# Optimization experiments

Hardware: AMD Instinct MI355X
Metric: run time of the kernel (lower is better)

## Reference

```python
import jax, jax.numpy as jnp
import numpy as np

N = 500_000
B = 4096
H = 256
NH = 4
D = H // NH


def setup_inputs() -> dict:
    key = jax.random.key(0)
    ks = jax.random.split(key, 9)
    node_feats = jax.random.normal(ks[0], (N, H), dtype=jnp.float32)
    g_feats = jax.random.normal(ks[1], (B, H), dtype=jnp.float32)
    degree = jax.random.uniform(ks[2], (N, 1), dtype=jnp.float32)
    seg = jnp.sort(jax.random.randint(ks[3], (N,), 0, B, dtype=jnp.int32))
    attn = jax.random.normal(ks[4], (1, NH, D), dtype=jnp.float32) * 0.1
    W1 = jax.random.normal(ks[5], (H, H), dtype=jnp.float32) * (1.0 / np.sqrt(H))
    b1 = jnp.zeros((H,), dtype=jnp.float32)
    W2 = jax.random.normal(ks[6], (H, H), dtype=jnp.float32) * (1.0 / np.sqrt(H))
    b2 = jnp.zeros((H,), dtype=jnp.float32)
    return {"node_feats": node_feats, "g_feats": g_feats, "degree": degree,
            "seg": seg, "attn": attn, "W1": W1, "b1": b1, "W2": W2, "b2": b2}


def reference(node_feats, g_feats, degree, seg, attn, W1, b1, W2, b2):
    nB, nH = g_feats.shape
    nD = nH // NH
    # broadcast graph feats to nodes + residual, split into heads: [N, NH, D]
    hv = (g_feats[seg] + node_feats).reshape(-1, NH, nD)
    # attention score per node per head: [N, NH]
    z = jnp.einsum('nhd,ohd->nh', hv, attn)
    z = z * degree  # degree [N,1] broadcasts over heads
    # per-graph (segment) softmax over nodes, per head
    zmax = jax.ops.segment_max(z, seg, num_segments=nB)  # [B, NH]
    zmax = jnp.where(jnp.isfinite(zmax), zmax, 0.0)       # guard empty graphs
    e = jnp.exp(z - zmax[seg])
    denom = jax.ops.segment_sum(e, seg, num_segments=nB)  # [B, NH]
    a = e / jnp.maximum(denom[seg], 1e-12)                 # [N, NH]
    # weighted segment sum of hv: [B, NH, D] -> [B, H]
    he = jax.ops.segment_sum(hv * a[:, :, None], seg, num_segments=nB)
    he = he.reshape(nB, nH)
    # lin1 (ReLU) then lin2 (no act), residual with g_feats
    h1 = jax.nn.relu(he @ W1.T + b1)
    h2 = h1 @ W2.T + b2
    return h2 + g_feats
```

## Files before the change

### kernel.cpp

```cpp
#include <hip/hip_runtime.h>
#include <math.h>

#define H 256
#define NHD 4
#define BM 8

typedef float f32x4 __attribute__((ext_vector_type(4)));

__global__ void transpose2_kernel(const float* __restrict__ W1,
                                  const float* __restrict__ W2,
                                  float* __restrict__ W1T,
                                  float* __restrict__ W2T) {
    __shared__ float tile[32][33];
    const int which = blockIdx.x >> 6;
    const float* in = which ? W2 : W1;
    float* out = which ? W2T : W1T;
    const int blk = blockIdx.x & 63;
    const int bx = blk & 7, by = blk >> 3;
    const int tx = threadIdx.x & 31, ty = threadIdx.x >> 5;
#pragma unroll
    for (int r = 0; r < 32; r += 8)
        tile[ty + r][tx] = in[(by * 32 + ty + r) * H + bx * 32 + tx];
    __syncthreads();
#pragma unroll
    for (int r = 0; r < 32; r += 8)
        out[(bx * 32 + ty + r) * H + by * 32 + tx] = tile[tx][ty + r];
}

__launch_bounds__(256, 8)
__global__ void pool_kernel(const float* __restrict__ node_feats,
                            const float* __restrict__ g_feats,
                            const float* __restrict__ degree,
                            const float* __restrict__ attn,
                            const int* __restrict__ seg,
                            int N,
                            float* __restrict__ he_out) {
    const int b = blockIdx.x;
    const int tid = threadIdx.x;
    const int wave = tid >> 6;
    const int lane = tid & 63;

    __shared__ int sb[2];
    if (tid < 2) {
        const int target = b + tid;
        int lo = 0, hi = N;
        while (lo < hi) {
            int mid = (lo + hi) >> 1;
            if (seg[mid] < target) lo = mid + 1; else hi = mid;
        }
        sb[tid] = lo;
    }
    __syncthreads();
    const int start = sb[0];
    const int end = sb[1];

    const float4 g4 = *reinterpret_cast<const float4*>(g_feats + (size_t)b * H + lane * 4);
    const float4 a4 = *reinterpret_cast<const float4*>(attn + lane * 4);

    float gz = g4.x * a4.x + g4.y * a4.y + g4.z * a4.z + g4.w * a4.w;
#pragma unroll
    for (int s = 1; s < 16; s <<= 1) gz += __shfl_xor(gz, s, 64);

    float m = -INFINITY, lsum = 0.0f;
    float4 acc = make_float4(0.f, 0.f, 0.f, 0.f);

    int n0 = start + wave * 4;
    for (; n0 + 4 <= end; n0 += 16) {
        const float* rp = node_feats + (size_t)n0 * H + lane * 4;
        f32x4 v0 = __builtin_nontemporal_load(reinterpret_cast<const f32x4*>(rp));
        f32x4 v1 = __builtin_nontemporal_load(reinterpret_cast<const f32x4*>(rp + H));
        f32x4 v2 = __builtin_nontemporal_load(reinterpret_cast<const f32x4*>(rp + 2 * H));
        f32x4 v3 = __builtin_nontemporal_load(reinterpret_cast<const f32x4*>(rp + 3 * H));
        const float d0 = degree[n0], d1 = degree[n0 + 1];
        const float d2 = degree[n0 + 2], d3 = degree[n0 + 3];

        float p0 = v0[0] * a4.x + v0[1] * a4.y + v0[2] * a4.z + v0[3] * a4.w;
        float p1 = v1[0] * a4.x + v1[1] * a4.y + v1[2] * a4.z + v1[3] * a4.w;
        float p2 = v2[0] * a4.x + v2[1] * a4.y + v2[2] * a4.z + v2[3] * a4.w;
        float p3 = v3[0] * a4.x + v3[1] * a4.y + v3[2] * a4.z + v3[3] * a4.w;
#pragma unroll
        for (int s = 1; s < 16; s <<= 1) {
            p0 += __shfl_xor(p0, s, 64);
            p1 += __shfl_xor(p1, s, 64);
            p2 += __shfl_xor(p2, s, 64);
            p3 += __shfl_xor(p3, s, 64);
        }
        const float z0 = (p0 + gz) * d0, z1 = (p1 + gz) * d1;
        const float z2 = (p2 + gz) * d2, z3 = (p3 + gz) * d3;

        const float mz = fmaxf(fmaxf(z0, z1), fmaxf(z2, z3));
        const float e0 = __expf(z0 - mz), e1 = __expf(z1 - mz);
        const float e2 = __expf(z2 - mz), e3 = __expf(z3 - mz);
        const float ls = e0 + e1 + e2 + e3;
        const float ax = e0 * v0[0] + e1 * v1[0] + e2 * v2[0] + e3 * v3[0] + ls * g4.x;
        const float ay = e0 * v0[1] + e1 * v1[1] + e2 * v2[1] + e3 * v3[1] + ls * g4.y;
        const float az = e0 * v0[2] + e1 * v1[2] + e2 * v2[2] + e3 * v3[2] + ls * g4.z;
        const float aw = e0 * v0[3] + e1 * v1[3] + e2 * v2[3] + e3 * v3[3] + ls * g4.w;

        const float mnew = fmaxf(m, mz);
        const float fo = __expf(m - mnew);
        const float fn = __expf(mz - mnew);
        lsum = lsum * fo + ls * fn;
        acc.x = acc.x * fo + ax * fn;
        acc.y = acc.y * fo + ay * fn;
        acc.z = acc.z * fo + az * fn;
        acc.w = acc.w * fo + aw * fn;
        m = mnew;
    }
    const int nend = (n0 + 4 < end) ? (n0 + 4) : end;
    for (int n = n0; n < nend; ++n) {
        const float* rp = node_feats + (size_t)n * H + lane * 4;
        f32x4 v = __builtin_nontemporal_load(reinterpret_cast<const f32x4*>(rp));
        float p = v[0] * a4.x + v[1] * a4.y + v[2] * a4.z + v[3] * a4.w;
#pragma unroll
        for (int s = 1; s < 16; s <<= 1) p += __shfl_xor(p, s, 64);
        const float z = (p + gz) * degree[n];
        const float mnew = fmaxf(m, z);
        const float fo = __expf(m - mnew);
        const float e = __expf(z - mnew);
        lsum = lsum * fo + e;
        acc.x = acc.x * fo + e * (v[0] + g4.x);
        acc.y = acc.y * fo + e * (v[1] + g4.y);
        acc.z = acc.z * fo + e * (v[2] + g4.z);
        acc.w = acc.w * fo + e * (v[3] + g4.w);
        m = mnew;
    }

    __shared__ float sm[4][NHD];
    __shared__ float sl[4][NHD];
    __shared__ float sacc[4][H];
    const int head = lane >> 4;
    if ((lane & 15) == 0) { sm[wave][head] = m; sl[wave][head] = lsum; }
    *reinterpret_cast<float4*>(&sacc[wave][lane * 4]) = acc;
    __syncthreads();

    const int h = tid >> 6;
    float mstar = fmaxf(fmaxf(sm[0][h], sm[1][h]), fmaxf(sm[2][h], sm[3][h]));
    if (!(mstar > -INFINITY)) mstar = 0.0f;
    float denom = 0.0f, hev = 0.0f;
#pragma unroll
    for (int w = 0; w < 4; ++w) {
        float fw = __expf(sm[w][h] - mstar);
        denom += sl[w][h] * fw;
        hev += sacc[w][tid] * fw;
    }
    he_out[(size_t)b * H + tid] = hev / fmaxf(denom, 1e-12f);
}

__launch_bounds__(256, 4)
__global__ void mlp_kernel(const float* __restrict__ he,
                           const float* __restrict__ W1T,
                           const float* __restrict__ b1,
                           const float* __restrict__ W2T,
                           const float* __restrict__ b2,
                           const float* __restrict__ g_feats,
                           float* __restrict__ out) {
    __shared__ float hbuf[BM][H];
    __shared__ float h1buf[BM][H];
    const int tid = threadIdx.x;
    const size_t row0 = (size_t)blockIdx.x * BM;

#pragma unroll
    for (int i = 0; i < BM; ++i)
        hbuf[i][tid] = he[(row0 + i) * H + tid];
    __syncthreads();

    float acc[BM];
#pragma unroll
    for (int i = 0; i < BM; ++i) acc[i] = 0.f;
    for (int k = 0; k < H; k += 4) {
        float w0 = W1T[(size_t)(k + 0) * H + tid];
        float w1 = W1T[(size_t)(k + 1) * H + tid];
        float w2 = W1T[(size_t)(k + 2) * H + tid];
        float w3 = W1T[(size_t)(k + 3) * H + tid];
#pragma unroll
        for (int i = 0; i < BM; ++i) {
            float4 hv = *reinterpret_cast<const float4*>(&hbuf[i][k]);
            acc[i] += hv.x * w0 + hv.y * w1 + hv.z * w2 + hv.w * w3;
        }
    }
    float bb1 = b1[tid];
#pragma unroll
    for (int i = 0; i < BM; ++i) h1buf[i][tid] = fmaxf(acc[i] + bb1, 0.f);
    __syncthreads();

#pragma unroll
    for (int i = 0; i < BM; ++i) acc[i] = 0.f;
    for (int k = 0; k < H; k += 4) {
        float w0 = W2T[(size_t)(k + 0) * H + tid];
        float w1 = W2T[(size_t)(k + 1) * H + tid];
        float w2 = W2T[(size_t)(k + 2) * H + tid];
        float w3 = W2T[(size_t)(k + 3) * H + tid];
#pragma unroll
        for (int i = 0; i < BM; ++i) {
            float4 hv = *reinterpret_cast<const float4*>(&h1buf[i][k]);
            acc[i] += hv.x * w0 + hv.y * w1 + hv.z * w2 + hv.w * w3;
        }
    }
    float bb2 = b2[tid];
#pragma unroll
    for (int i = 0; i < BM; ++i)
        out[(row0 + i) * H + tid] = acc[i] + bb2 + g_feats[(row0 + i) * H + tid];
}

extern "C" void kernel_launch(void* const* d_in, const int* in_sizes, int n_in,
                              void* d_out, int out_size, void* d_ws, size_t ws_size,
                              hipStream_t stream) {
    const float* node_feats = (const float*)d_in[0];
    const float* g_feats    = (const float*)d_in[1];
    const float* degree     = (const float*)d_in[2];
    const int*   seg        = (const int*)d_in[3];
    const float* attn       = (const float*)d_in[4];
    const float* W1         = (const float*)d_in[5];
    const float* b1         = (const float*)d_in[6];
    const float* W2         = (const float*)d_in[7];
    const float* b2         = (const float*)d_in[8];
    float* out = (float*)d_out;

    const int N = in_sizes[3];
    const int B = in_sizes[1] / H;

    char* ws = (char*)d_ws;
    float* W1T = (float*)ws;
    float* W2T = (float*)(ws + H * H * 4);
    float* he  = (float*)(ws + 2 * H * H * 4);

    transpose2_kernel<<<128, 256, 0, stream>>>(W1, W2, W1T, W2T);
    pool_kernel<<<B, 256, 0, stream>>>(node_feats, g_feats, degree, attn, seg, N, he);
    mlp_kernel<<<B / BM, 256, 0, stream>>>(he, W1T, b1, W2T, b2, g_feats, out);
}
```

Before: 139.1 us.

## Precompute segment bounds in a separate kernel and split-K the MLP across waves

Adds a kernel that writes per-graph start offsets from the sorted segment ids, so each pool block reads two integers instead of running two serial binary searches before any work. The MLP kernel now gives each wave a quarter of the K dimension and has each thread compute four output columns, then reduces the partial sums through shared memory. The goal is more register-level reuse of the loaded weights and more independent FMA chains. The cost is an extra launch, a larger shared-memory buffer and an added reduction step with barriers.

```diff
diff --git a/kernel.cpp b/kernel.cpp
--- a/kernel.cpp
+++ b/kernel.cpp
@@ -6,6 +6,23 @@
 #define BM 8
 
 typedef float f32x4 __attribute__((ext_vector_type(4)));
+
+__global__ void seg_bounds_kernel(const int* __restrict__ seg,
+                                  int* __restrict__ seg_start,
+                                  int N, int B) {
+    int n = blockIdx.x * blockDim.x + threadIdx.x;
+    if (n >= N) return;
+    int s = seg[n];
+    if (n == 0) {
+        for (int b = 0; b <= s; ++b) seg_start[b] = 0;
+    } else {
+        int sp = seg[n - 1];
+        for (int b = sp + 1; b <= s; ++b) seg_start[b] = n;
+    }
+    if (n == N - 1) {
+        for (int b = s + 1; b <= B; ++b) seg_start[b] = N;
+    }
+}
 
 __global__ void transpose2_kernel(const float* __restrict__ W1,
                                   const float* __restrict__ W2,
@@ -32,27 +49,14 @@
                             const float* __restrict__ g_feats,
                             const float* __restrict__ degree,
                             const float* __restrict__ attn,
-                            const int* __restrict__ seg,
-                            int N,
+                            const int* __restrict__ seg_start,
                             float* __restrict__ he_out) {
     const int b = blockIdx.x;
     const int tid = threadIdx.x;
     const int wave = tid >> 6;
     const int lane = tid & 63;
-
-    __shared__ int sb[2];
-    if (tid < 2) {
-        const int target = b + tid;
-        int lo = 0, hi = N;
-        while (lo < hi) {
-            int mid = (lo + hi) >> 1;
-            if (seg[mid] < target) lo = mid + 1; else hi = mid;
-        }
-        sb[tid] = lo;
-    }
-    __syncthreads();
-    const int start = sb[0];
-    const int end = sb[1];
+    const int start = seg_start[b];
+    const int end = seg_start[b + 1];
 
     const float4 g4 = *reinterpret_cast<const float4*>(g_feats + (size_t)b * H + lane * 4);
     const float4 a4 = *reinterpret_cast<const float4*>(attn + lane * 4);
@@ -156,8 +160,10 @@
                            const float* __restrict__ g_feats,
                            float* __restrict__ out) {
     __shared__ float hbuf[BM][H];
-    __shared__ float h1buf[BM][H];
+    __shared__ float pacc[4][BM][H];
     const int tid = threadIdx.x;
+    const int q = tid >> 6;
+    const int l = tid & 63;
     const size_t row0 = (size_t)blockIdx.x * BM;
 
 #pragma unroll
@@ -165,42 +171,62 @@
         hbuf[i][tid] = he[(row0 + i) * H + tid];
     __syncthreads();
 
-    float acc[BM];
-#pragma unroll
-    for (int i = 0; i < BM; ++i) acc[i] = 0.f;
-    for (int k = 0; k < H; k += 4) {
-        float w0 = W1T[(size_t)(k + 0) * H + tid];
-        float w1 = W1T[(size_t)(k + 1) * H + tid];
-        float w2 = W1T[(size_t)(k + 2) * H + tid];
-        float w3 = W1T[(size_t)(k + 3) * H + tid];
-#pragma unroll
-        for (int i = 0; i < BM; ++i) {
-            float4 hv = *reinterpret_cast<const float4*>(&hbuf[i][k]);
-            acc[i] += hv.x * w0 + hv.y * w1 + hv.z * w2 + hv.w * w3;
+#pragma unroll
+    for (int layer = 0; layer < 2; ++layer) {
+        const float* WT = layer ? W2T : W1T;
+        float acc[BM][4];
+#pragma unroll
+        for (int i = 0; i < BM; ++i)
+#pragma unroll
+            for (int j = 0; j < 4; ++j) acc[i][j] = 0.f;
+
+        const int k0 = q * 64;
+        for (int s = 0; s < 64; s += 4) {
+            const int k = k0 + s;
+            float w[4][4];
+#pragma unroll
+            for (int kk = 0; kk < 4; ++kk)
+#pragma unroll
+                for (int j = 0; j < 4; ++j)
+                    w[kk][j] = WT[(size_t)(k + kk) * H + l + 64 * j];
+#pragma unroll
+            for (int i = 0; i < BM; ++i) {
+                const f32x4 hv = *reinterpret_cast<const f32x4*>(&hbuf[i][k]);
+#pragma unroll
+                for (int j = 0; j < 4; ++j) {
+                    acc[i][j] = __builtin_fmaf(hv[0], w[0][j], acc[i][j]);
+                    acc[i][j] = __builtin_fmaf(hv[1], w[1][j], acc[i][j]);
+                    acc[i][j] = __builtin_fmaf(hv[2], w[2][j], acc[i][j]);
+                    acc[i][j] = __builtin_fmaf(hv[3], w[3][j], acc[i][j]);
+                }
+            }
         }
-    }
-    float bb1 = b1[tid];
-#pragma unroll
-    for (int i = 0; i < BM; ++i) h1buf[i][tid] = fmaxf(acc[i] + bb1, 0.f);
-    __syncthreads();
-
-#pragma unroll
-    for (int i = 0; i < BM; ++i) acc[i] = 0.f;
-    for (int k = 0; k < H; k += 4) {
-        float w0 = W2T[(size_t)(k + 0) * H + tid];
-        float w1 = W2T[(size_t)(k + 1) * H + tid];
-        float w2 = W2T[(size_t)(k + 2) * H + tid];
-        float w3 = W2T[(size_t)(k + 3) * H + tid];
-#pragma unroll
-        for (int i = 0; i < BM; ++i) {
-            float4 hv = *reinterpret_cast<const float4*>(&h1buf[i][k]);
-            acc[i] += hv.x * w0 + hv.y * w1 + hv.z * w2 + hv.w * w3;
+#pragma unroll
+        for (int i = 0; i < BM; ++i)
+#pragma unroll
+            for (int j = 0; j < 4; ++j)
+                pacc[q][i][l + 64 * j] = acc[i][j];
+        __syncthreads();
+
+        const int i = tid >> 5;
+        const int cbase = tid & 31;
+        if (layer == 0) {
+#pragma unroll
+            for (int mm = 0; mm < 8; ++mm) {
+                const int c = cbase + 32 * mm;
+                float v = pacc[0][i][c] + pacc[1][i][c] + pacc[2][i][c] + pacc[3][i][c];
+                hbuf[i][c] = fmaxf(v + b1[c], 0.f);
+            }
+        } else {
+#pragma unroll
+            for (int mm = 0; mm < 8; ++mm) {
+                const int c = cbase + 32 * mm;
+                float v = pacc[0][i][c] + pacc[1][i][c] + pacc[2][i][c] + pacc[3][i][c];
+                out[(row0 + i) * H + c] = v + b2[c] + g_feats[(row0 + i) * H + c];
+            }
         }
-    }
-    float bb2 = b2[tid];
-#pragma unroll
-    for (int i = 0; i < BM; ++i)
-        out[(row0 + i) * H + tid] = acc[i] + bb2 + g_feats[(row0 + i) * H + tid];
+        __syncthreads();
+    }
 }
 
 extern "C" void kernel_launch(void* const* d_in, const int* in_sizes, int n_in,
@@ -221,11 +247,13 @@
     const int B = in_sizes[1] / H;
 
     char* ws = (char*)d_ws;
-    float* W1T = (float*)ws;
-    float* W2T = (float*)(ws + H * H * 4);
-    float* he  = (float*)(ws + 2 * H * H * 4);
-
+    int*   seg_start = (int*)ws;
+    float* W1T = (float*)(ws + 32768);
+    float* W2T = (float*)(ws + 32768 + H * H * 4);
+    float* he  = (float*)(ws + 32768 + 2 * H * H * 4);
+
+    seg_bounds_kernel<<<(N + 255) / 256, 256, 0, stream>>>(seg, seg_start, N, B);
     transpose2_kernel<<<128, 256, 0, stream>>>(W1, W2, W1T, W2T);
-    pool_kernel<<<B, 256, 0, stream>>>(node_feats, g_feats, degree, attn, seg, N, he);
+    pool_kernel<<<B, 256, 0, stream>>>(node_feats, g_feats, degree, attn, seg_start, he);
     mlp_kernel<<<B / BM, 256, 0, stream>>>(he, W1T, b1, W2T, b2, g_feats, out);
 }
```

Measured after the change: 112.5 us. -19.1%, faster.
